# Kernel tuning notes

Hardware: AMD Instinct MI355X
Metric: run time of the kernel (lower is better)

The kernel has to match this reference:

```python
import jax, jax.numpy as jnp
import numpy as np

WS = 7      # window size
SS = 3      # shift size = WS // 2
NH = 12     # num heads
EPS = 1e-5  # LayerNorm eps


def _ln(x, g, b):
    m = jnp.mean(x, axis=-1, keepdims=True)
    v = jnp.var(x, axis=-1, keepdims=True)
    return (x - m) * jax.lax.rsqrt(v + EPS) * g + b


def _rel_index(ws):
    # relative position index (N, N), N = ws*ws (static, numpy)
    coords = np.stack(np.meshgrid(np.arange(ws), np.arange(ws), indexing='ij')).reshape(2, -1)
    rel = (coords[:, :, None] - coords[:, None, :]).transpose(1, 2, 0).copy()
    rel[:, :, 0] += ws - 1
    rel[:, :, 1] += ws - 1
    rel[:, :, 0] *= 2 * ws - 1
    return rel.sum(-1)


def _attn_mask(H, W, ws, ss):
    # SW-MSA mask (nW, N, N): -100 where tokens come from different shifted regions
    img = np.zeros((H, W), np.float32)
    cnt = 0
    sls = (slice(0, -ws), slice(-ws, -ss), slice(-ss, None))
    for hs in sls:
        for wsl in sls:
            img[hs, wsl] = cnt
            cnt += 1
    win = img.reshape(H // ws, ws, W // ws, ws).transpose(0, 2, 1, 3).reshape(-1, ws * ws)
    d = win[:, None, :] - win[:, :, None]
    return np.where(d != 0, -100.0, 0.0).astype(np.float32)


def _forward(x, rel_bias_table, qkv_w, qkv_b, proj_w, proj_b,
             norm1_w, norm1_b, norm2_w, norm2_b,
             mlp_w1, mlp_b1, mlp_w2, mlp_b2, h, w):
    B, L, C = x.shape
    ws, ss, nH = WS, SS, NH
    hd = C // nH
    N = ws * ws
    scale = hd ** -0.5
    nWh, nWw = h // ws, w // ws
    nW = nWh * nWw

    shortcut = x
    y = _ln(x, norm1_w, norm1_b).reshape(B, h, w, C)
    # cyclic shift (SW-MSA)
    y = jnp.roll(y, (-ss, -ss), axis=(1, 2))
    # window partition -> (B*nW, N, C)
    y = y.reshape(B, nWh, ws, nWw, ws, C).transpose(0, 1, 3, 2, 4, 5).reshape(-1, N, C)

    qkv = (y @ qkv_w + qkv_b).reshape(-1, N, 3, nH, hd).transpose(2, 0, 3, 1, 4)
    q, k, v = qkv[0] * scale, qkv[1], qkv[2]  # (Bw, nH, N, hd)

    attn = jnp.einsum('bhnd,bhmd->bhnm', q, k)  # (Bw, nH, N, N)
    # learned relative position bias
    idx = jnp.asarray(_rel_index(ws))  # (N, N)
    bias = rel_bias_table[idx].transpose(2, 0, 1)[None]  # (1, nH, N, N)
    attn = attn + bias
    # shifted-window mask
    mask = jnp.asarray(_attn_mask(h, w, ws, ss))  # (nW, N, N)
    attn = attn.reshape(B, nW, nH, N, N) + mask[None, :, None]
    attn = jax.nn.softmax(attn.reshape(-1, nH, N, N), axis=-1)

    out = jnp.einsum('bhnm,bhmd->bhnd', attn, v).transpose(0, 2, 1, 3).reshape(-1, N, C)
    out = out @ proj_w + proj_b
    # window reverse + un-shift
    out = out.reshape(B, nWh, nWw, ws, ws, C).transpose(0, 1, 3, 2, 4, 5).reshape(B, h, w, C)
    out = jnp.roll(out, (ss, ss), axis=(1, 2)).reshape(B, L, C)

    x = shortcut + out
    y2 = _ln(x, norm2_w, norm2_b)
    mlp = jax.nn.gelu(y2 @ mlp_w1 + mlp_b1, approximate=False) @ mlp_w2 + mlp_b2
    return x + mlp


def setup_inputs() -> dict:
    key = jax.random.key(0)
    ks = jax.random.split(key, 8)
    B, H, W, C = 32, 56, 56, 384
    hid = int(C * 4.0)
    ws, nH = WS, NH
    inp = {
        'x': jax.random.normal(ks[0], (B, H * W, C), jnp.float32),
        'rel_bias_table': 0.02 * jax.random.normal(ks[1], ((2 * ws - 1) * (2 * ws - 1), nH), jnp.float32),
        'qkv_w': 0.02 * jax.random.normal(ks[2], (C, 3 * C), jnp.float32),
        'qkv_b': jnp.zeros((3 * C,), jnp.float32),
        'proj_w': 0.02 * jax.random.normal(ks[3], (C, C), jnp.float32),
        'proj_b': jnp.zeros((C,), jnp.float32),
        'norm1_w': jnp.ones((C,), jnp.float32),
        'norm1_b': jnp.zeros((C,), jnp.float32),
        'norm2_w': jnp.ones((C,), jnp.float32),
        'norm2_b': jnp.zeros((C,), jnp.float32),
        'mlp_w1': 0.02 * jax.random.normal(ks[4], (C, hid), jnp.float32),
        'mlp_b1': jnp.zeros((hid,), jnp.float32),
        'mlp_w2': 0.02 * jax.random.normal(ks[5], (hid, C), jnp.float32),
        'mlp_b2': jnp.zeros((C,), jnp.float32),
        'h': H,
        'w': W,
    }
    return inp


def reference(x, rel_bias_table, qkv_w, qkv_b, proj_w, proj_b,
              norm1_w, norm1_b, norm2_w, norm2_b,
              mlp_w1, mlp_b1, mlp_w2, mlp_b2, h, w):
    return _forward(x, rel_bias_table, qkv_w, qkv_b, proj_w, proj_b,
                    norm1_w, norm1_b, norm2_w, norm2_b,
                    mlp_w1, mlp_b1, mlp_w2, mlp_b2, h, w)
```

## Files before the change

kernel.cpp:

```cpp
#include <hip/hip_runtime.h>

typedef unsigned short u16;
typedef unsigned int u32;
typedef short s8v __attribute__((ext_vector_type(8)));
typedef float f4 __attribute__((ext_vector_type(4)));

#define GL16(g, l) __builtin_amdgcn_global_load_lds((const __attribute__((address_space(1))) u32*)(g), (__attribute__((address_space(3))) u32*)(l), 16, 0, 0)

__device__ __forceinline__ u16 f2bf(float f){
  u32 u = __builtin_bit_cast(u32, f);
  u32 r = u + 0x7fffu + ((u >> 16) & 1u);
  return (u16)(r >> 16);
}
__device__ __forceinline__ float bf2f(u16 u){
  u32 x = ((u32)u) << 16;
  return __builtin_bit_cast(float, x);
}

__device__ __forceinline__ u32 pk_bf16(float lo, float hi){
  u32 r;
  asm("v_cvt_pk_bf16_f32 %0, %1, %2" : "=v"(r) : "v"(lo), "v"(hi));
  return r;
}

__device__ __forceinline__ float gelu_f(float x){
  float y = fabsf(x) * 0.70710678118654752f;
  float t = __builtin_amdgcn_rcpf(1.f + 0.3275911f*y);
  float p = ((((1.061405429f*t - 1.453152027f)*t + 1.421413741f)*t - 0.284496736f)*t + 0.254829592f)*t;
  float er = 1.f - p*__expf(-y*y);
  er = copysignf(er, x);
  return 0.5f*x*(1.f + er);
}

__device__ __forceinline__ int win_to_src(int orow){
  int wi = orow / 49;
  int n  = orow - wi*49;
  int b  = wi >> 6;
  int wq = wi & 63;
  int wh = wq >> 3, ww = wq & 7;
  int r = n / 7, c = n - r*7;
  int hh = wh*7 + r + 3; if (hh >= 56) hh -= 56;
  int wp = ww*7 + c + 3; if (wp >= 56) wp -= 56;
  return (b*56 + hh)*56 + wp;
}

__global__ void sentinel_kernel(float* o){ o[0] = 1.0e9f; }

__global__ void transpose_cast(const float* __restrict__ in, u16* __restrict__ out,
                               int K, int N, float scale, int scale_lim){
  __shared__ float tile[16][17];
  int kb = blockIdx.x*16, nb = blockIdx.y*16;
  int tx = threadIdx.x, ty = threadIdx.y;
  int k = kb + ty, n = nb + tx;
  tile[ty][tx] = (k < K && n < N) ? in[(size_t)k*N + n] : 0.f;
  __syncthreads();
  int on = nb + ty, ok = kb + tx;
  if (on < N && ok < K){
    float v = tile[tx][ty];
    if (on < scale_lim) v *= scale;
    out[(size_t)on*K + ok] = f2bf(v);
  }
}

__global__ void scale_bias(const float* __restrict__ in, float* __restrict__ out,
                           int n, float s, int lim){
  int i = blockIdx.x*256 + threadIdx.x;
  if (i < n) out[i] = in[i] * (i < lim ? s : 1.f);
}

__global__ void build_biasmask(const float* __restrict__ table, u16* __restrict__ bm){
  int wq = blockIdx.x, h = blockIdx.y;
  int wh = wq >> 3, ww = wq & 7;
  u16* o = bm + (size_t)(wq*12 + h) * 4096;
  for (int i = threadIdx.x; i < 4096; i += 256){
    int m = i >> 6, n = i & 63;
    float v;
    if (m < 49 && n < 49){
      int rm = m/7, cm = m - rm*7;
      int rn = n/7, cn = n - rn*7;
      int idx = (rm - rn + 6)*13 + (cm - cn + 6);
      v = table[idx*12 + h];
      int ym = wh*7 + rm, xm = ww*7 + cm;
      int yn = wh*7 + rn, xn = ww*7 + cn;
      int lm = (ym < 49 ? 0 : (ym < 53 ? 1 : 2))*3 + (xm < 49 ? 0 : (xm < 53 ? 1 : 2));
      int ln = (yn < 49 ? 0 : (yn < 53 ? 1 : 2))*3 + (xn < 49 ? 0 : (xn < 53 ? 1 : 2));
      if (lm != ln) v += -100.f;
    } else {
      v = -1e9f;
    }
    o[i] = f2bf(v);
  }
}

template<bool GATHER>
__global__ __launch_bounds__(256) void ln_kernel(const float* __restrict__ x,
    const float* __restrict__ g, const float* __restrict__ b,
    u16* __restrict__ y, int nrows)
{
  int row = blockIdx.x*4 + (threadIdx.x >> 6);
  int lane = threadIdx.x & 63;
  if (row >= nrows) return;
  int src = GATHER ? win_to_src(row) : row;
  const float* xr = x + (size_t)src*384;
  float v[6];
  float s = 0.f, s2 = 0.f;
  #pragma unroll
  for (int p = 0; p < 3; p++){
    float2 t = *(const float2*)(xr + p*128 + lane*2);
    v[p*2] = t.x; v[p*2+1] = t.y;
    s += t.x + t.y; s2 += t.x*t.x + t.y*t.y;
  }
  #pragma unroll
  for (int off = 32; off; off >>= 1){
    s  += __shfl_xor(s,  off);
    s2 += __shfl_xor(s2, off);
  }
  float mean = s * (1.f/384.f);
  float var  = s2 * (1.f/384.f) - mean*mean;
  float rs   = rsqrtf(var + 1e-5f);
  u16* yr = y + (size_t)row*384;
  #pragma unroll
  for (int p = 0; p < 3; p++){
    int c = p*128 + lane*2;
    float a0 = (v[p*2]   - mean)*rs*g[c]   + b[c];
    float a1 = (v[p*2+1] - mean)*rs*g[c+1] + b[c+1];
    *(u32*)(yr + c) = pk_bf16(a0, a1);
  }
}

template<int MODE, int NF>
__global__ __launch_bounds__(256) void gemm_bf16(
    const u16* __restrict__ A, const u16* __restrict__ Bt,
    const float* __restrict__ bias, const float* __restrict__ resid,
    void* __restrict__ outp, int K, int N, int gn)
{
  constexpr int TN = NF * 32;
  __shared__ u16 smem[6*4096];
  const int tid  = threadIdx.x;
  const int lane = tid & 63, wv = tid >> 6;
  const int wr = wv >> 1, wc = wv & 1;
  const int l15 = lane & 15, lhi = lane >> 4;
  const int key = (l15 >> 1) & 3;

  int total = gridDim.x;
  int flat  = blockIdx.x;
  int swz   = flat;
  if ((total & 7) == 0){
    int cpx = total >> 3;
    swz = (flat & 7)*cpx + (flat >> 3);
  }
  int bm = swz / gn, bn = swz - bm*gn;
  const size_t m0 = (size_t)bm * 128;
  const int n0 = bn * TN;

  f4 acc[4][NF] = {};

  auto stage = [&](int buf, int kt){
    #pragma unroll
    for (int it = 0; it < 2; it++){
      int c = it*256 + tid;
      int row = c >> 2;
      int col = ((c & 3) ^ ((c >> 3) & 3)) * 8;
      const u16* ga = A + (m0 + (size_t)row)*K + kt*32 + col;
      GL16(ga, &smem[buf*4096 + (it*256 + wv*64)*8]);
    }
    #pragma unroll
    for (int it = 0; it < 2; it++){
      int c = it*256 + tid;
      int row = c >> 2;
      int col = ((c & 3) ^ ((c >> 3) & 3)) * 8;
      const u16* gb = Bt + ((size_t)n0 + row)*K + kt*32 + col;
      GL16(gb, &smem[12288 + buf*4096 + (it*256 + wv*64)*8]);
    }
  };

  const int nk = K >> 5;
  stage(0, 0);
  stage(1, 1);
  int cur = 0;
  for (int kt = 0; kt < nk; kt++){
    if (kt + 2 < nk){
      int nb = cur + 2; if (nb >= 3) nb -= 3;
      stage(nb, kt + 2);
      asm volatile("s_waitcnt vmcnt(8)" ::: "memory");
    } else if (kt + 1 < nk){
      asm volatile("s_waitcnt vmcnt(4)" ::: "memory");
    } else {
      asm volatile("s_waitcnt vmcnt(0)" ::: "memory");
    }
    __builtin_amdgcn_s_barrier();

    s8v a[4], bb[NF];
    #pragma unroll
    for (int mi = 0; mi < 4; mi++)
      a[mi] = *(const s8v*)&smem[cur*4096 + (wr*64 + mi*16 + l15)*32 + ((lhi ^ key))*8];
    #pragma unroll
    for (int ni = 0; ni < NF; ni++)
      bb[ni] = *(const s8v*)&smem[12288 + cur*4096 + (wc*NF*16 + ni*16 + l15)*32 + ((lhi ^ key))*8];
    #pragma unroll
    for (int mi = 0; mi < 4; mi++)
      #pragma unroll
      for (int ni = 0; ni < NF; ni++)
        acc[mi][ni] = __builtin_amdgcn_mfma_f32_16x16x32_bf16(bb[ni], a[mi], acc[mi][ni], 0, 0, 0);

    asm volatile("s_waitcnt lgkmcnt(0)" ::: "memory");
    __builtin_amdgcn_s_barrier();
    cur = (cur == 2) ? 0 : cur + 1;
  }

  if constexpr (MODE == 0 || MODE == 2){
    u16* tile = smem;
    #pragma unroll
    for (int mi = 0; mi < 4; mi++){
      int ml = wr*64 + mi*16 + l15;
      #pragma unroll
      for (int ni = 0; ni < NF; ni++){
        int nl = wc*NF*16 + ni*16 + lhi*4;
        f4 v = acc[mi][ni];
        float4 b4 = *(const float4*)(bias + n0 + nl);
        v[0] += b4.x; v[1] += b4.y; v[2] += b4.z; v[3] += b4.w;
        u32 p0, p1;
        if constexpr (MODE == 2){
          p0 = pk_bf16(gelu_f(v[0]), gelu_f(v[1]));
          p1 = pk_bf16(gelu_f(v[2]), gelu_f(v[3]));
        } else {
          p0 = pk_bf16(v[0], v[1]);
          p1 = pk_bf16(v[2], v[3]);
        }
        *(u32*)&tile[ml*136 + nl]     = p0;
        *(u32*)&tile[ml*136 + nl + 2] = p1;
      }
    }
    __syncthreads();
    int rr = tid >> 4;
    int cc = (tid & 15) * 8;
    #pragma unroll
    for (int pass = 0; pass < 8; pass++){
      int row = rr + pass*16;
      uint4 val = *(const uint4*)&tile[row*136 + cc];
      *(uint4*)((u16*)outp + ((size_t)((int)m0 + row))*N + n0 + cc) = val;
    }
  } else {
    #pragma unroll
    for (int mi = 0; mi < 4; mi++){
      int m = (int)m0 + wr*64 + mi*16 + l15;
      int src = 0;
      if constexpr (MODE == 1) src = win_to_src(m);
      #pragma unroll
      for (int ni = 0; ni < NF; ni++){
        int n = n0 + wc*NF*16 + ni*16 + lhi*4;
        f4 v = acc[mi][ni];
        float4 b4 = *(const float4*)(bias + n);
        v[0] += b4.x; v[1] += b4.y; v[2] += b4.z; v[3] += b4.w;
        if constexpr (MODE == 1){
          const float4 r4 = *(const float4*)(resid + (size_t)src*384 + n);
          float4 o4; o4.x = v[0]+r4.x; o4.y = v[1]+r4.y; o4.z = v[2]+r4.z; o4.w = v[3]+r4.w;
          *(float4*)((float*)outp + (size_t)src*384 + n) = o4;
        } else {
          float4* o = (float4*)((float*)outp + (size_t)m*N + n);
          float4 c4 = *o;
          c4.x += v[0]; c4.y += v[1]; c4.z += v[2]; c4.w += v[3];
          *o = c4;
        }
      }
    }
  }
}

__global__ __launch_bounds__(256) void attn_kernel(
    const u16* __restrict__ qkv, const u16* __restrict__ bm, u16* __restrict__ ao)
{
  const int wi = blockIdx.x;
  const int hg = blockIdx.y;
  const int wv = threadIdx.x >> 6, lane = threadIdx.x & 63;
  const int h = hg*4 + wv;
  const int l15 = lane & 15, lhi = lane >> 4;
  const int wq = wi & 63;

  __shared__ u16 Plds[4][64*72];
  __shared__ u16 Vlds[4][32*72];

  const size_t base = (size_t)wi * 49 * 1152;
  s8v z8 = (s8v)0;

  #pragma unroll
  for (int i = 0; i < 4; i++){
    int n  = i*16 + (lane >> 2);
    int d8 = (lane & 3)*8;
    s8v v = (n < 49) ? *(const s8v*)&qkv[base + (size_t)n*1152 + 768 + h*32 + d8] : z8;
    #pragma unroll
    for (int j = 0; j < 8; j++)
      Vlds[wv][(d8 + j)*72 + n] = (u16)v[j];
  }

  s8v aQ[4], bK[4];
  #pragma unroll
  for (int mi = 0; mi < 4; mi++){
    int rowq = mi*16 + l15;
    aQ[mi] = (rowq < 49) ? *(const s8v*)&qkv[base + (size_t)rowq*1152 +   0 + h*32 + lhi*8] : z8;
    bK[mi] = (rowq < 49) ? *(const s8v*)&qkv[base + (size_t)rowq*1152 + 384 + h*32 + lhi*8] : z8;
  }
  f4 zf = {0.f, 0.f, 0.f, 0.f};
  f4 s[4][4];
  #pragma unroll
  for (int mi = 0; mi < 4; mi++)
    #pragma unroll
    for (int ni = 0; ni < 4; ni++)
      s[mi][ni] = __builtin_amdgcn_mfma_f32_16x16x32_bf16(aQ[mi], bK[ni], zf, 0, 0, 0);

  const u16* bmp = bm + (size_t)(wq*12 + h) * 4096;
  #pragma unroll
  for (int mi = 0; mi < 4; mi++)
    #pragma unroll
    for (int ni = 0; ni < 4; ni++)
      #pragma unroll
      for (int r = 0; r < 4; r++){
        int m = mi*16 + lhi*4 + r, n = ni*16 + l15;
        s[mi][ni][r] += bf2f(bmp[m*64 + n]);
      }

  #pragma unroll
  for (int mi = 0; mi < 4; mi++){
    #pragma unroll
    for (int r = 0; r < 4; r++){
      float mx = fmaxf(fmaxf(s[mi][0][r], s[mi][1][r]), fmaxf(s[mi][2][r], s[mi][3][r]));
      mx = fmaxf(mx, __shfl_xor(mx, 1));
      mx = fmaxf(mx, __shfl_xor(mx, 2));
      mx = fmaxf(mx, __shfl_xor(mx, 4));
      mx = fmaxf(mx, __shfl_xor(mx, 8));
      float sum = 0.f;
      #pragma unroll
      for (int ni = 0; ni < 4; ni++){
        float p = __expf(s[mi][ni][r] - mx);
        s[mi][ni][r] = p; sum += p;
      }
      sum += __shfl_xor(sum, 1);
      sum += __shfl_xor(sum, 2);
      sum += __shfl_xor(sum, 4);
      sum += __shfl_xor(sum, 8);
      float inv = 1.f / sum;
      #pragma unroll
      for (int ni = 0; ni < 4; ni++) s[mi][ni][r] *= inv;
    }
  }

  #pragma unroll
  for (int mi = 0; mi < 4; mi++)
    #pragma unroll
    for (int ni = 0; ni < 4; ni++)
      #pragma unroll
      for (int r = 0; r < 4; r++){
        int m = mi*16 + lhi*4 + r, n = ni*16 + l15;
        Plds[wv][m*72 + n] = f2bf(s[mi][ni][r]);
      }
  __syncthreads();

  f4 o[4][2] = {};
  #pragma unroll
  for (int ks = 0; ks < 2; ks++){
    s8v aP[4], bV[2];
    #pragma unroll
    for (int mi = 0; mi < 4; mi++)
      aP[mi] = *(const s8v*)&Plds[wv][(mi*16 + l15)*72 + ks*32 + lhi*8];
    #pragma unroll
    for (int di = 0; di < 2; di++)
      bV[di] = *(const s8v*)&Vlds[wv][(di*16 + l15)*72 + ks*32 + lhi*8];
    #pragma unroll
    for (int mi = 0; mi < 4; mi++)
      #pragma unroll
      for (int di = 0; di < 2; di++)
        o[mi][di] = __builtin_amdgcn_mfma_f32_16x16x32_bf16(aP[mi], bV[di], o[mi][di], 0, 0, 0);
  }

  #pragma unroll
  for (int mi = 0; mi < 4; mi++)
    #pragma unroll
    for (int di = 0; di < 2; di++)
      #pragma unroll
      for (int r = 0; r < 4; r++){
        int m = mi*16 + lhi*4 + r;
        if (m < 49){
          int d = di*16 + l15;
          ao[((size_t)wi*49 + m)*384 + h*32 + d] = f2bf(o[mi][di][r]);
        }
      }
}

extern "C" void kernel_launch(void* const* d_in, const int* in_sizes, int n_in,
                              void* d_out, int out_size, void* d_ws, size_t ws_size,
                              hipStream_t stream)
{
  const float* x      = (const float*)d_in[0];
  const float* table  = (const float*)d_in[1];
  const float* qkv_w  = (const float*)d_in[2];
  const float* qkv_b  = (const float*)d_in[3];
  const float* proj_w = (const float*)d_in[4];
  const float* proj_b = (const float*)d_in[5];
  const float* n1w    = (const float*)d_in[6];
  const float* n1b    = (const float*)d_in[7];
  const float* n2w    = (const float*)d_in[8];
  const float* n2b    = (const float*)d_in[9];
  const float* w1     = (const float*)d_in[10];
  const float* b1     = (const float*)d_in[11];
  const float* w2     = (const float*)d_in[12];
  const float* b2     = (const float*)d_in[13];
  float* out = (float*)d_out;

  const size_t M = 100352;
  const float SC = 0.17677669529663689f;

  const size_t R1 = M * 1536 * 2;
  const size_t R2 = M * 384 * 2;
  const size_t R3 = (size_t)64*12*64*64*2;
  const size_t WT = (size_t)(1152*384 + 384*384 + 1536*384 + 384*1536) * 2;
  const size_t BB = 1152 * 4;
  const size_t needed = R1 + R2 + R3 + WT + BB;
  if (ws_size < needed){
    sentinel_kernel<<<1, 1, 0, stream>>>(out);
    return;
  }

  char* p = (char*)d_ws;
  u16*   qkvbuf = (u16*)p;
  u16*   ybuf   = (u16*)(p + R1);
  u16*   bmbuf  = (u16*)(p + R1 + R2);
  u16*   qkvT   = (u16*)(p + R1 + R2 + R3);
  u16*   projT  = qkvT  + (size_t)1152*384;
  u16*   w1T    = projT + (size_t)384*384;
  u16*   w2T    = w1T   + (size_t)1536*384;
  float* qkvb_s = (float*)(p + R1 + R2 + R3 + WT);

  transpose_cast<<<dim3(24, 72),  dim3(16,16), 0, stream>>>(qkv_w,  qkvT, 384, 1152, SC, 384);
  transpose_cast<<<dim3(24, 24),  dim3(16,16), 0, stream>>>(proj_w, projT, 384, 384, 1.f, 0);
  transpose_cast<<<dim3(24, 96),  dim3(16,16), 0, stream>>>(w1,     w1T,  384, 1536, 1.f, 0);
  transpose_cast<<<dim3(96, 24),  dim3(16,16), 0, stream>>>(w2,     w2T,  1536, 384, 1.f, 0);
  scale_bias<<<5, 256, 0, stream>>>(qkv_b, qkvb_s, 1152, SC, 384);
  build_biasmask<<<dim3(64, 12), 256, 0, stream>>>(table, bmbuf);

  ln_kernel<true><<<M/4, 256, 0, stream>>>(x, n1w, n1b, ybuf, (int)M);

  gemm_bf16<0,4><<<784*9, 256, 0, stream>>>(ybuf, qkvT, qkvb_s, nullptr, qkvbuf, 384, 1152, 9);

  attn_kernel<<<dim3(2048, 3), 256, 0, stream>>>(qkvbuf, bmbuf, ybuf);

  gemm_bf16<1,4><<<784*3, 256, 0, stream>>>(ybuf, projT, proj_b, x, out, 384, 384, 3);

  ln_kernel<false><<<M/4, 256, 0, stream>>>(out, n2w, n2b, ybuf, (int)M);

  gemm_bf16<2,4><<<784*12, 256, 0, stream>>>(ybuf, w1T, b1, nullptr, qkvbuf, 384, 1536, 12);

  gemm_bf16<3,4><<<784*3, 256, 0, stream>>>(qkvbuf, w2T, b2, nullptr, out, 1536, 384, 3);
}
```

Before: 941.2 us.

## Enlarge GEMM tiles to 256x128 and restructure the pipeline barrier

The GEMM block tile grows from 128x128 to 256x128, so each wave computes a 128x64 sub-tile with 8x4 MFMA accumulators and the grid halves. The K loop now waits and barriers once at the top, then issues the next prefetch after the barrier, removing the second per-iteration barrier. The larger tile raises data reuse per LDS load, but it also raises register and LDS use (72KB shared, launch_bounds 2), which can lower occupancy. The epilogue tile staging in LDS now covers 256 rows with a 136 stride, and this must fit inside the 36864-element buffer.

```diff
diff --git a/kernel.cpp b/kernel.cpp
--- a/kernel.cpp
+++ b/kernel.cpp
@@ -128,17 +128,16 @@
   }
 }
 
-template<int MODE, int NF>
-__global__ __launch_bounds__(256) void gemm_bf16(
+template<int MODE>
+__global__ __launch_bounds__(256, 2) void gemm_bf16(
     const u16* __restrict__ A, const u16* __restrict__ Bt,
     const float* __restrict__ bias, const float* __restrict__ resid,
     void* __restrict__ outp, int K, int N, int gn)
 {
-  constexpr int TN = NF * 32;
-  __shared__ u16 smem[6*4096];
+  __shared__ u16 smem[36864];
   const int tid  = threadIdx.x;
   const int lane = tid & 63, wv = tid >> 6;
-  const int wr = wv >> 1, wc = wv & 1;
+  const int wm = wv >> 1, wn = wv & 1;
   const int l15 = lane & 15, lhi = lane >> 4;
   const int key = (l15 >> 1) & 3;
 
@@ -150,19 +149,19 @@
     swz = (flat & 7)*cpx + (flat >> 3);
   }
   int bm = swz / gn, bn = swz - bm*gn;
-  const size_t m0 = (size_t)bm * 128;
-  const int n0 = bn * TN;
-
-  f4 acc[4][NF] = {};
+  const size_t m0 = (size_t)bm * 256;
+  const int n0 = bn * 128;
+
+  f4 acc[8][4] = {};
 
   auto stage = [&](int buf, int kt){
     #pragma unroll
-    for (int it = 0; it < 2; it++){
+    for (int it = 0; it < 4; it++){
       int c = it*256 + tid;
       int row = c >> 2;
       int col = ((c & 3) ^ ((c >> 3) & 3)) * 8;
       const u16* ga = A + (m0 + (size_t)row)*K + kt*32 + col;
-      GL16(ga, &smem[buf*4096 + (it*256 + wv*64)*8]);
+      GL16(ga, &smem[buf*8192 + (it*256 + wv*64)*8]);
     }
     #pragma unroll
     for (int it = 0; it < 2; it++){
@@ -170,7 +169,7 @@
       int row = c >> 2;
       int col = ((c & 3) ^ ((c >> 3) & 3)) * 8;
       const u16* gb = Bt + ((size_t)n0 + row)*K + kt*32 + col;
-      GL16(gb, &smem[12288 + buf*4096 + (it*256 + wv*64)*8]);
+      GL16(gb, &smem[24576 + buf*4096 + (it*256 + wv*64)*8]);
     }
   };
 
@@ -179,43 +178,44 @@
   stage(1, 1);
   int cur = 0;
   for (int kt = 0; kt < nk; kt++){
+    if (kt + 1 < nk){
+      asm volatile("s_waitcnt vmcnt(6)" ::: "memory");
+    } else {
+      asm volatile("s_waitcnt vmcnt(0)" ::: "memory");
+    }
+    asm volatile("s_waitcnt lgkmcnt(0)" ::: "memory");
+    __builtin_amdgcn_s_barrier();
     if (kt + 2 < nk){
       int nb = cur + 2; if (nb >= 3) nb -= 3;
       stage(nb, kt + 2);
-      asm volatile("s_waitcnt vmcnt(8)" ::: "memory");
-    } else if (kt + 1 < nk){
-      asm volatile("s_waitcnt vmcnt(4)" ::: "memory");
-    } else {
-      asm volatile("s_waitcnt vmcnt(0)" ::: "memory");
-    }
-    __builtin_amdgcn_s_barrier();
-
-    s8v a[4], bb[NF];
-    #pragma unroll
-    for (int mi = 0; mi < 4; mi++)
-      a[mi] = *(const s8v*)&smem[cur*4096 + (wr*64 + mi*16 + l15)*32 + ((lhi ^ key))*8];
-    #pragma unroll
-    for (int ni = 0; ni < NF; ni++)
-      bb[ni] = *(const s8v*)&smem[12288 + cur*4096 + (wc*NF*16 + ni*16 + l15)*32 + ((lhi ^ key))*8];
-    #pragma unroll
-    for (int mi = 0; mi < 4; mi++)
-      #pragma unroll
-      for (int ni = 0; ni < NF; ni++)
+    }
+
+    s8v a[8], bb[4];
+    #pragma unroll
+    for (int mi = 0; mi < 8; mi++)
+      a[mi] = *(const s8v*)&smem[cur*8192 + (wm*128 + mi*16 + l15)*32 + ((lhi ^ key))*8];
+    #pragma unroll
+    for (int ni = 0; ni < 4; ni++)
+      bb[ni] = *(const s8v*)&smem[24576 + cur*4096 + (wn*64 + ni*16 + l15)*32 + ((lhi ^ key))*8];
+    #pragma unroll
+    for (int mi = 0; mi < 8; mi++)
+      #pragma unroll
+      for (int ni = 0; ni < 4; ni++)
         acc[mi][ni] = __builtin_amdgcn_mfma_f32_16x16x32_bf16(bb[ni], a[mi], acc[mi][ni], 0, 0, 0);
 
+    cur = (cur == 2) ? 0 : cur + 1;
+  }
+
+  if constexpr (MODE == 0 || MODE == 2){
     asm volatile("s_waitcnt lgkmcnt(0)" ::: "memory");
     __builtin_amdgcn_s_barrier();
-    cur = (cur == 2) ? 0 : cur + 1;
-  }
-
-  if constexpr (MODE == 0 || MODE == 2){
     u16* tile = smem;
     #pragma unroll
-    for (int mi = 0; mi < 4; mi++){
-      int ml = wr*64 + mi*16 + l15;
-      #pragma unroll
-      for (int ni = 0; ni < NF; ni++){
-        int nl = wc*NF*16 + ni*16 + lhi*4;
+    for (int mi = 0; mi < 8; mi++){
+      int ml = wm*128 + mi*16 + l15;
+      #pragma unroll
+      for (int ni = 0; ni < 4; ni++){
+        int nl = wn*64 + ni*16 + lhi*4;
         f4 v = acc[mi][ni];
         float4 b4 = *(const float4*)(bias + n0 + nl);
         v[0] += b4.x; v[1] += b4.y; v[2] += b4.z; v[3] += b4.w;
@@ -235,20 +235,20 @@
     int rr = tid >> 4;
     int cc = (tid & 15) * 8;
     #pragma unroll
-    for (int pass = 0; pass < 8; pass++){
+    for (int pass = 0; pass < 16; pass++){
       int row = rr + pass*16;
       uint4 val = *(const uint4*)&tile[row*136 + cc];
       *(uint4*)((u16*)outp + ((size_t)((int)m0 + row))*N + n0 + cc) = val;
     }
   } else {
     #pragma unroll
-    for (int mi = 0; mi < 4; mi++){
-      int m = (int)m0 + wr*64 + mi*16 + l15;
+    for (int mi = 0; mi < 8; mi++){
+      int m = (int)m0 + wm*128 + mi*16 + l15;
       int src = 0;
       if constexpr (MODE == 1) src = win_to_src(m);
       #pragma unroll
-      for (int ni = 0; ni < NF; ni++){
-        int n = n0 + wc*NF*16 + ni*16 + lhi*4;
+      for (int ni = 0; ni < 4; ni++){
+        int n = n0 + wn*64 + ni*16 + lhi*4;
         f4 v = acc[mi][ni];
         float4 b4 = *(const float4*)(bias + n);
         v[0] += b4.x; v[1] += b4.y; v[2] += b4.z; v[3] += b4.w;
@@ -439,15 +439,15 @@
 
   ln_kernel<true><<<M/4, 256, 0, stream>>>(x, n1w, n1b, ybuf, (int)M);
 
-  gemm_bf16<0,4><<<784*9, 256, 0, stream>>>(ybuf, qkvT, qkvb_s, nullptr, qkvbuf, 384, 1152, 9);
+  gemm_bf16<0><<<392*9, 256, 0, stream>>>(ybuf, qkvT, qkvb_s, nullptr, qkvbuf, 384, 1152, 9);
 
   attn_kernel<<<dim3(2048, 3), 256, 0, stream>>>(qkvbuf, bmbuf, ybuf);
 
-  gemm_bf16<1,4><<<784*3, 256, 0, stream>>>(ybuf, projT, proj_b, x, out, 384, 384, 3);
+  gemm_bf16<1><<<392*3, 256, 0, stream>>>(ybuf, projT, proj_b, x, out, 384, 384, 3);
 
   ln_kernel<false><<<M/4, 256, 0, stream>>>(out, n2w, n2b, ybuf, (int)M);
 
-  gemm_bf16<2,4><<<784*12, 256, 0, stream>>>(ybuf, w1T, b1, nullptr, qkvbuf, 384, 1536, 12);
-
-  gemm_bf16<3,4><<<784*3, 256, 0, stream>>>(qkvbuf, w2T, b2, nullptr, out, 1536, 384, 3);
-}
+  gemm_bf16<2><<<392*12, 256, 0, stream>>>(ybuf, w1T, b1, nullptr, qkvbuf, 384, 1536, 12);
+
+  gemm_bf16<3><<<392*3, 256, 0, stream>>>(qkvbuf, w2T, b2, nullptr, out, 1536, 384, 3);
+}
```

Result: faster. 890.7 us (-5.4%).
